# Performance work log

Measured on AMD Instinct MI355X. Metric: run time of the kernel, lower is better.

## Reference

```python
import jax, jax.numpy as jnp
import numpy as np

H = 16        # num_attention_heads
HS = 128      # head_size
ROT = 32      # rotary_ndims (partial RoPE, NeoX rotary_pct=0.25)
BASE = 10000.0


def _rope_cache(seq_len):
    inv_freq = 1.0 / (BASE ** (jnp.arange(0, ROT, 2, dtype=jnp.float32) / ROT))
    t = jnp.arange(seq_len, dtype=jnp.float32)
    freqs = jnp.outer(t, inv_freq)                      # [s, ROT/2]
    emb = jnp.concatenate([freqs, freqs], axis=-1)      # [s, ROT]
    return jnp.cos(emb), jnp.sin(emb)


def _rotate_half(x):
    x1, x2 = jnp.split(x, 2, axis=-1)
    return jnp.concatenate([-x2, x1], axis=-1)


def setup_inputs() -> dict:
    key = jax.random.key(0)
    k1, k2, k3 = jax.random.split(key, 3)
    B, S, D = 2, 2048, 2048
    hidden_states = jax.random.normal(k1, (B, S, D), dtype=jnp.float32)
    position_ids = jnp.broadcast_to(jnp.arange(S, dtype=jnp.int64 if jax.config.jax_enable_x64 else jnp.int32), (B, S))
    W_qkv = jax.random.normal(k2, (D, 3 * H * HS), dtype=jnp.float32) * 0.02
    b_qkv = jnp.zeros((3 * H * HS,), dtype=jnp.float32)
    W_dense = jax.random.normal(k3, (H * HS, D), dtype=jnp.float32) * 0.02
    b_dense = jnp.zeros((D,), dtype=jnp.float32)
    return {"hidden_states": hidden_states, "position_ids": position_ids,
            "W_qkv": W_qkv, "b_qkv": b_qkv, "W_dense": W_dense, "b_dense": b_dense}


def reference(hidden_states, position_ids, W_qkv, b_qkv, W_dense, b_dense):
    B, S, D = hidden_states.shape
    # fused QKV projection, NeoX layout: [b, s, h, 3*hs]
    qkv = (hidden_states @ W_qkv + b_qkv).reshape(B, S, H, 3 * HS)
    q = qkv[..., :HS]            # [b, s, h, hs]
    k = qkv[..., HS:2 * HS]
    v = qkv[..., 2 * HS:]

    # partial rotary embedding on first ROT dims
    cos, sin = _rope_cache(S)                       # [s, ROT]
    cos = cos[position_ids][:, :, None, :]          # [b, s, 1, ROT]
    sin = sin[position_ids][:, :, None, :]
    q_rot, q_pass = q[..., :ROT], q[..., ROT:]
    k_rot, k_pass = k[..., :ROT], k[..., ROT:]
    q_rot = q_rot * cos + _rotate_half(q_rot) * sin
    k_rot = k_rot * cos + _rotate_half(k_rot) * sin
    q = jnp.concatenate([q_rot, q_pass], axis=-1)
    k = jnp.concatenate([k_rot, k_pass], axis=-1)

    # scaled dot-product attention (no mask, as in the source SDPA call)
    scale = 1.0 / jnp.sqrt(jnp.asarray(HS, dtype=q.dtype))
    scores = jnp.einsum('bqhd,bkhd->bhqk', q, k) * scale   # [b, h, s, s]
    attn = jax.nn.softmax(scores, axis=-1)
    out = jnp.einsum('bhqk,bkhd->bqhd', attn, v)            # [b, s, h, hs]
    out = out.reshape(B, S, H * HS)                         # 'b h d n -> b d (h n)'
    return out @ W_dense + b_dense
```

## Files before the change

### kernel.cpp

```cpp
#include <hip/hip_runtime.h>

typedef short bf16x8 __attribute__((ext_vector_type(8)));
typedef float f32x4 __attribute__((ext_vector_type(4)));

#define S_LEN 2048
#define NHEAD 16
#define HSZ 128

__device__ __forceinline__ float bf2f(ushort u) {
    union { unsigned int i; float f; } x; x.i = ((unsigned int)u) << 16; return x.f;
}
__device__ __forceinline__ ushort f2bf(float f) {
    union { float f; unsigned int i; } x; x.f = f;
    unsigned int r = (x.i + 0x7FFFu + ((x.i >> 16) & 1u)) >> 16;
    return (ushort)r;
}

__device__ __forceinline__ void gload16(const ushort* g, ushort* l) {
    __builtin_amdgcn_global_load_lds(
        (const __attribute__((address_space(1))) unsigned int*)g,
        (__attribute__((address_space(3))) unsigned int*)l,
        16, 0, 0);
}

__global__ void cast_kernel(const float* __restrict__ in, ushort* __restrict__ out, int n4) {
    int i = blockIdx.x * 256 + threadIdx.x;
    if (i >= n4) return;
    float4 v = ((const float4*)in)[i];
    ushort4 r;
    r.x = f2bf(v.x); r.y = f2bf(v.y); r.z = f2bf(v.z); r.w = f2bf(v.w);
    ((ushort4*)out)[i] = r;
}

__global__ void transpose_cast(const float* __restrict__ W, ushort* __restrict__ WT,
                               int K, int N) {
    __shared__ float tile[32][33];
    int n = blockIdx.x * 32 + threadIdx.x;
    #pragma unroll
    for (int j = 0; j < 32; j += 8) {
        int k = blockIdx.y * 32 + threadIdx.y + j;
        tile[threadIdx.y + j][threadIdx.x] = W[(size_t)k * N + n];
    }
    __syncthreads();
    int k2 = blockIdx.y * 32 + threadIdx.x;
    #pragma unroll
    for (int j = 0; j < 32; j += 8) {
        int n2 = blockIdx.x * 32 + threadIdx.y + j;
        WT[(size_t)n2 * K + k2] = f2bf(tile[threadIdx.x][threadIdx.y + j]);
    }
}

template <int EPI>
__global__ __launch_bounds__(512, 2) void gemm256(
    const ushort* __restrict__ A, const ushort* __restrict__ Bt,
    const float* __restrict__ bias, float* __restrict__ Cout, int Kdim, int Ndim,
    ushort* __restrict__ q_out, ushort* __restrict__ k_out, ushort* __restrict__ v_out) {
    __shared__ __align__(16) ushort lA[4][8192];
    __shared__ __align__(16) ushort lB[4][8192];
    const int tid = threadIdx.x;
    const int m0 = blockIdx.y * 256, n0 = blockIdx.x * 256;
    const int lane = tid & 63, wid = tid >> 6;
    const int wm = wid >> 2, wn = wid & 3;
    const int lm = lane & 15, quad = lane >> 4;
    const int srow = tid >> 2;
    const int g8 = ((tid & 3) ^ ((tid >> 3) & 3)) * 8;
    const int wb = wid * 512;
    const int ch8 = (quad ^ ((lm >> 1) & 3)) * 8;
    const int aoff = (wm * 128 + lm) * 32 + ch8;
    const int boff = (wn * 64 + lm) * 32 + ch8;

    const ushort* pA = A + (size_t)(m0 + srow) * Kdim + g8;
    const ushort* pB = Bt + (size_t)(n0 + srow) * Kdim + g8;
    const size_t rhalf = (size_t)128 * Kdim;

    f32x4 acc[8][4];
    #pragma unroll
    for (int i = 0; i < 8; ++i)
        #pragma unroll
        for (int j = 0; j < 4; ++j) acc[i][j] = (f32x4){0.f, 0.f, 0.f, 0.f};

    const int T = Kdim >> 5;
    gload16(pA,              lA[0] + wb);
    gload16(pA + rhalf,      lA[0] + 4096 + wb);
    gload16(pB,              lB[0] + wb);
    gload16(pB + rhalf,      lB[0] + 4096 + wb);
    gload16(pA + 32,         lA[1] + wb);
    gload16(pA + 32 + rhalf, lA[1] + 4096 + wb);
    gload16(pB + 32,         lB[1] + wb);
    gload16(pB + 32 + rhalf, lB[1] + 4096 + wb);
    asm volatile("s_waitcnt vmcnt(4)" ::: "memory");
    asm volatile("s_barrier" ::: "memory");

    for (int t = 0; t < T; ++t) {
        const ushort* la = lA[t & 3];
        const ushort* lb = lB[t & 3];
        bf16x8 af[4], bfr[4];
        #pragma unroll
        for (int mt = 0; mt < 4; ++mt) af[mt] = *(const bf16x8*)(la + aoff + mt * 512);
        #pragma unroll
        for (int nt = 0; nt < 4; ++nt) bfr[nt] = *(const bf16x8*)(lb + boff + nt * 512);
        if (t + 2 < T) {
            ushort* da = lA[(t + 2) & 3];
            const ushort* sa = pA + (size_t)(t + 2) * 32;
            gload16(sa,         da + wb);
            gload16(sa + rhalf, da + 4096 + wb);
        }
        asm volatile("s_barrier" ::: "memory");
        __builtin_amdgcn_s_setprio(1);
        #pragma unroll
        for (int mt = 0; mt < 4; ++mt)
            #pragma unroll
            for (int nt = 0; nt < 4; ++nt)
                acc[mt][nt] = __builtin_amdgcn_mfma_f32_16x16x32_bf16(
                    af[mt], bfr[nt], acc[mt][nt], 0, 0, 0);
        __builtin_amdgcn_s_setprio(0);

        bf16x8 af2[4];
        #pragma unroll
        for (int mt = 0; mt < 4; ++mt) af2[mt] = *(const bf16x8*)(la + aoff + 2048 + mt * 512);
        if (t + 2 < T) {
            ushort* db = lB[(t + 2) & 3];
            const ushort* sb = pB + (size_t)(t + 2) * 32;
            gload16(sb,         db + wb);
            gload16(sb + rhalf, db + 4096 + wb);
        }
        asm volatile("s_barrier" ::: "memory");
        __builtin_amdgcn_s_setprio(1);
        #pragma unroll
        for (int mt = 0; mt < 4; ++mt)
            #pragma unroll
            for (int nt = 0; nt < 4; ++nt)
                acc[4 + mt][nt] = __builtin_amdgcn_mfma_f32_16x16x32_bf16(
                    af2[mt], bfr[nt], acc[4 + mt][nt], 0, 0, 0);
        __builtin_amdgcn_s_setprio(0);
        if (t + 2 < T) asm volatile("s_waitcnt vmcnt(4)" ::: "memory");
        else           asm volatile("s_waitcnt vmcnt(0)" ::: "memory");
        asm volatile("s_barrier" ::: "memory");
    }

    #pragma unroll
    for (int mt = 0; mt < 8; ++mt) {
        #pragma unroll
        for (int nt = 0; nt < 4; ++nt) {
            f32x4 c = acc[mt][nt];
            int gn = n0 + wn * 64 + nt * 16 + lm;
            float bv = bias[gn];
            #pragma unroll
            for (int i = 0; i < 4; ++i) {
                int gm = m0 + wm * 128 + mt * 16 + quad * 4 + i;
                float v = c[i] + bv;
                if (EPI == 0) {
                    int h = gn / 384, r = gn - h * 384;
                    int tt = r >> 7, d = r & 127;
                    int b = gm >> 11, s = gm & 2047;
                    ushort bb = f2bf(v);
                    if (tt == 0) {
                        q_out[((size_t)(b * NHEAD + h) * S_LEN + s) * HSZ + d] = bb;
                    } else if (tt == 1) {
                        k_out[((size_t)(b * NHEAD + h) * S_LEN + s) * HSZ + d] = bb;
                    } else {
                        v_out[((size_t)(b * NHEAD + h) * HSZ + d) * S_LEN + s] = bb;
                    }
                } else {
                    Cout[(size_t)gm * Ndim + gn] = v;
                }
            }
        }
    }
}

template <int EPI>
__global__ __launch_bounds__(256) void gemm128(
    const ushort* __restrict__ A, const ushort* __restrict__ Bt,
    const float* __restrict__ bias, float* __restrict__ Cout, int Kdim, int Ndim,
    ushort* __restrict__ q_out, ushort* __restrict__ k_out, ushort* __restrict__ v_out) {
    __shared__ __align__(16) ushort lA[2][128 * 32];
    __shared__ __align__(16) ushort lB[2][128 * 32];
    const int tid = threadIdx.x;
    const int m0 = blockIdx.y * 128, n0 = blockIdx.x * 128;
    const int lane = tid & 63, wid = tid >> 6;
    const int wm = wid >> 1, wn = wid & 1, lm = lane & 15, quad = lane >> 4;
    const int srow = tid >> 2;
    const int gc = (tid & 3) ^ ((tid >> 3) & 3);
    const int wb8 = (wid << 6) * 8;
    const int cs = (quad ^ ((lm >> 1) & 3)) * 8;

    const ushort* pA = A  + (size_t)(m0 + srow) * Kdim + gc * 8;
    const ushort* pB = Bt + (size_t)(n0 + srow) * Kdim + gc * 8;
    const size_t rhalf = (size_t)64 * Kdim;

    const int fA = (wm * 64 + lm) * 32;
    const int fB = (wn * 64 + lm) * 32;

    f32x4 acc[16];
    #pragma unroll
    for (int i = 0; i < 16; ++i) acc[i] = (f32x4){0.f, 0.f, 0.f, 0.f};

    const int T = Kdim >> 5;
    gload16(pA,         lA[0] + wb8);
    gload16(pA + rhalf, lA[0] + 2048 + wb8);
    gload16(pB,         lB[0] + wb8);
    gload16(pB + rhalf, lB[0] + 2048 + wb8);
    pA += 32; pB += 32;

    for (int t = 0; t < T; ++t) {
        __syncthreads();
        const ushort* la = lA[t & 1];
        const ushort* lb = lB[t & 1];
        if (t + 1 < T) {
            ushort* da = lA[(t + 1) & 1];
            ushort* db = lB[(t + 1) & 1];
            gload16(pA,         da + wb8);
            gload16(pA + rhalf, da + 2048 + wb8);
            gload16(pB,         db + wb8);
            gload16(pB + rhalf, db + 2048 + wb8);
            pA += 32; pB += 32;
        }
        bf16x8 af[4], bfr[4];
        #pragma unroll
        for (int t4 = 0; t4 < 4; ++t4) {
            af[t4]  = *(const bf16x8*)(la + fA + t4 * 512 + cs);
            bfr[t4] = *(const bf16x8*)(lb + fB + t4 * 512 + cs);
        }
        #pragma unroll
        for (int mt = 0; mt < 4; ++mt)
            #pragma unroll
            for (int nt = 0; nt < 4; ++nt)
                acc[mt * 4 + nt] = __builtin_amdgcn_mfma_f32_16x16x32_bf16(
                    af[mt], bfr[nt], acc[mt * 4 + nt], 0, 0, 0);
    }

    #pragma unroll
    for (int mt = 0; mt < 4; ++mt) {
        #pragma unroll
        for (int nt = 0; nt < 4; ++nt) {
            f32x4 c = acc[mt * 4 + nt];
            int gn = n0 + wn * 64 + nt * 16 + lm;
            float bv = bias[gn];
            #pragma unroll
            for (int i = 0; i < 4; ++i) {
                int gm = m0 + wm * 64 + mt * 16 + quad * 4 + i;
                float v = c[i] + bv;
                if (EPI == 0) {
                    int h = gn / 384, r = gn - h * 384;
                    int t = r >> 7, d = r & 127;
                    int b = gm >> 11, s = gm & 2047;
                    ushort bb = f2bf(v);
                    if (t == 0) {
                        q_out[((size_t)(b * NHEAD + h) * S_LEN + s) * HSZ + d] = bb;
                    } else if (t == 1) {
                        k_out[((size_t)(b * NHEAD + h) * S_LEN + s) * HSZ + d] = bb;
                    } else {
                        v_out[((size_t)(b * NHEAD + h) * HSZ + d) * S_LEN + s] = bb;
                    }
                } else {
                    Cout[(size_t)gm * Ndim + gn] = v;
                }
            }
        }
    }
}

__global__ void rope_kernel(ushort* __restrict__ Qr, ushort* __restrict__ Kr,
                            const int* __restrict__ pos_ids) {
    int idx = blockIdx.x * 256 + threadIdx.x;
    int j = idx & 15;
    int row = idx >> 4;
    int s = row & 2047;
    int bh = row >> 11;
    int b = bh >> 4;
    int pos = pos_ids[b * S_LEN + s];
    float inv = exp2f((float)j * -0.8304820237218405f);
    float th = (float)pos * inv;
    float sn, c;
    sincosf(th, &sn, &c);
    size_t base = (size_t)row * HSZ;
    {
        float x1 = bf2f(Qr[base + j]), x2 = bf2f(Qr[base + j + 16]);
        Qr[base + j]      = f2bf(x1 * c - x2 * sn);
        Qr[base + j + 16] = f2bf(x2 * c + x1 * sn);
    }
    {
        float x1 = bf2f(Kr[base + j]), x2 = bf2f(Kr[base + j + 16]);
        Kr[base + j]      = f2bf(x1 * c - x2 * sn);
        Kr[base + j + 16] = f2bf(x2 * c + x1 * sn);
    }
}

__global__ __launch_bounds__(256, 2) void attn_mfma(
    const ushort* __restrict__ Q, const ushort* __restrict__ K,
    const ushort* __restrict__ Vt, ushort* __restrict__ O) {
    __shared__ __align__(16) ushort lQ[128 * 136];
    __shared__ __align__(16) ushort lK[2][32 * 128];
    __shared__ __align__(16) ushort lVt[2][128 * 32];
    __shared__ __align__(16) ushort lP[4 * 32 * 40];

    const int tid = threadIdx.x;
    const int wid = tid >> 6, lane = tid & 63;
    const int L = lane & 15, quad = lane >> 4;
    const int bh = blockIdx.y;
    const int q0 = blockIdx.x * 128;
    const int wq0 = wid * 32;
    const size_t base = (size_t)bh * S_LEN * HSZ;
    const ushort* Qb = Q + base + (size_t)q0 * HSZ;
    const ushort* Kb = K + base;
    const ushort* Vb = Vt + base;
    ushort* lPw = lP + wid * (32 * 40);

    #pragma unroll
    for (int p = 0; p < 8; ++p) {
        int idx = tid + p * 256;
        int row = idx >> 4, ch = idx & 15;
        uint4 v = ((const uint4*)Qb)[idx];
        *(uint4*)(lQ + row * 136 + ch * 8) = v;
    }
    __syncthreads();

    bf16x8 qf[2][4];
    #pragma unroll
    for (int qs = 0; qs < 2; ++qs)
        #pragma unroll
        for (int dc = 0; dc < 4; ++dc)
            qf[qs][dc] = *(const bf16x8*)(lQ + (wq0 + qs * 16 + L) * 136 + dc * 32 + quad * 8);

    int kx[4];
    #pragma unroll
    for (int dc = 0; dc < 4; ++dc) kx[dc] = (((dc * 4 + quad) ^ (L & 7))) * 8;
    const int vx = (quad ^ ((L >> 1) & 3)) * 8;

    const int li0 = tid, li1 = tid + 256;
    const int ub0 = ((tid & 192)) * 8, ub1 = ((tid & 192) + 256) * 8;
    const int kr0 = li0 >> 4, kg0 = (li0 & 15) ^ (kr0 & 7);
    const int kr1 = li1 >> 4, kg1 = (li1 & 15) ^ (kr1 & 7);
    const int vd0 = li0 >> 2, vg0 = (li0 & 3) ^ ((vd0 >> 1) & 3);
    const int vd1 = li1 >> 2, vg1 = (li1 & 3) ^ ((vd1 >> 1) & 3);

    f32x4 acc_o[8][2];
    #pragma unroll
    for (int dt = 0; dt < 8; ++dt)
        #pragma unroll
        for (int qs = 0; qs < 2; ++qs) acc_o[dt][qs] = (f32x4){0.f, 0.f, 0.f, 0.f};
    float lacc[2] = {0.f, 0.f};
    const float scale = 0.08838834764831845f;
    const float SHIFT = 12.0f;

    {
        gload16(Kb + (size_t)kr0 * 128 + kg0 * 8, lK[0] + ub0);
        gload16(Kb + (size_t)kr1 * 128 + kg1 * 8, lK[0] + ub1);
        gload16(Vb + (size_t)vd0 * 2048 + vg0 * 8, lVt[0] + ub0);
        gload16(Vb + (size_t)vd1 * 2048 + vg1 * 8, lVt[0] + ub1);
    }

    for (int kt = 0; kt < S_LEN / 32; ++kt) {
        __syncthreads();
        const int cur = kt & 1;
        const ushort* lKc = lK[cur];
        const ushort* lVc = lVt[cur];
        if (kt + 1 < S_LEN / 32) {
            ushort* dK = lK[cur ^ 1];
            ushort* dV = lVt[cur ^ 1];
            int kb = (kt + 1) * 32;
            gload16(Kb + (size_t)(kb + kr0) * 128 + kg0 * 8, dK + ub0);
            gload16(Kb + (size_t)(kb + kr1) * 128 + kg1 * 8, dK + ub1);
            gload16(Vb + (size_t)vd0 * 2048 + kb + vg0 * 8, dV + ub0);
            gload16(Vb + (size_t)vd1 * 2048 + kb + vg1 * 8, dV + ub1);
        }

        f32x4 sa[2][2];
        #pragma unroll
        for (int t = 0; t < 2; ++t)
            #pragma unroll
            for (int qs = 0; qs < 2; ++qs) sa[t][qs] = (f32x4){0.f, 0.f, 0.f, 0.f};
        #pragma unroll
        for (int t = 0; t < 2; ++t)
            #pragma unroll
            for (int dc = 0; dc < 4; ++dc) {
                bf16x8 kf = *(const bf16x8*)(lKc + (t * 16 + L) * 128 + kx[dc]);
                sa[t][0] = __builtin_amdgcn_mfma_f32_16x16x32_bf16(kf, qf[0][dc], sa[t][0], 0, 0, 0);
                sa[t][1] = __builtin_amdgcn_mfma_f32_16x16x32_bf16(kf, qf[1][dc], sa[t][1], 0, 0, 0);
            }

        #pragma unroll
        for (int t = 0; t < 2; ++t)
            #pragma unroll
            for (int qs = 0; qs < 2; ++qs) {
                #pragma unroll
                for (int r = 0; r < 4; ++r) {
                    float pv = __expf(fmaf(sa[t][qs][r], scale, -SHIFT));
                    lacc[qs] += pv;
                    sa[t][qs][r] = pv;
                }
                ushort4 u;
                u.x = f2bf(sa[t][qs][0]);
                u.y = f2bf(sa[t][qs][1]);
                u.z = f2bf(sa[t][qs][2]);
                u.w = f2bf(sa[t][qs][3]);
                *(ushort4*)(lPw + (qs * 16 + L) * 40 + t * 16 + quad * 4) = u;
            }
        __asm__ volatile("s_waitcnt lgkmcnt(0)" ::: "memory");

        bf16x8 pf0 = *(const bf16x8*)(lPw + L * 40 + quad * 8);
        bf16x8 pf1 = *(const bf16x8*)(lPw + (16 + L) * 40 + quad * 8);
        #pragma unroll
        for (int dt = 0; dt < 8; ++dt) {
            bf16x8 vf = *(const bf16x8*)(lVc + (dt * 16 + L) * 32 + vx);
            acc_o[dt][0] = __builtin_amdgcn_mfma_f32_16x16x32_bf16(vf, pf0, acc_o[dt][0], 0, 0, 0);
            acc_o[dt][1] = __builtin_amdgcn_mfma_f32_16x16x32_bf16(vf, pf1, acc_o[dt][1], 0, 0, 0);
        }
    }

    const int b = bh >> 4, h = bh & 15;
    #pragma unroll
    for (int qs = 0; qs < 2; ++qs) {
        float l = lacc[qs];
        l += __shfl_xor(l, 16);
        l += __shfl_xor(l, 32);
        float inv = 1.f / l;
        size_t row = ((size_t)(b * S_LEN + q0 + wq0 + qs * 16 + L)) * (NHEAD * HSZ) + h * HSZ;
        #pragma unroll
        for (int dt = 0; dt < 8; ++dt) {
            ushort4 u;
            u.x = f2bf(acc_o[dt][qs][0] * inv);
            u.y = f2bf(acc_o[dt][qs][1] * inv);
            u.z = f2bf(acc_o[dt][qs][2] * inv);
            u.w = f2bf(acc_o[dt][qs][3] * inv);
            *(ushort4*)(O + row + dt * 16 + quad * 4) = u;
        }
    }
}

extern "C" void kernel_launch(void* const* d_in, const int* in_sizes, int n_in,
                              void* d_out, int out_size, void* d_ws, size_t ws_size,
                              hipStream_t stream) {
    const float* hidden = (const float*)d_in[0];
    const int*   pos    = (const int*)d_in[1];
    const float* Wqkv   = (const float*)d_in[2];
    const float* bqkv   = (const float*)d_in[3];
    const float* Wd     = (const float*)d_in[4];
    const float* bd     = (const float*)d_in[5];

    char* ws = (char*)d_ws;
    ushort* hA  = (ushort*)ws;
    ushort* WqT = (ushort*)(ws + 16777216ull);
    ushort* WdT = (ushort*)(ws + 41943040ull);
    ushort* Qb  = (ushort*)(ws + 50331648ull);
    ushort* Kb  = (ushort*)(ws + 67108864ull);
    ushort* Vb  = (ushort*)(ws + 83886080ull);

    cast_kernel<<<dim3(8192), dim3(256), 0, stream>>>(hidden, hA, 2097152);
    transpose_cast<<<dim3(192, 64), dim3(32, 8), 0, stream>>>(Wqkv, WqT, 2048, 6144);
    transpose_cast<<<dim3(64, 64), dim3(32, 8), 0, stream>>>(Wd, WdT, 2048, 2048);

    gemm256<0><<<dim3(24, 16), dim3(512), 0, stream>>>(hA, WqT, bqkv, nullptr, 2048, 6144,
                                                       Qb, Kb, Vb);
    rope_kernel<<<dim3(4096), dim3(256), 0, stream>>>(Qb, Kb, pos);

    ushort* Obuf = hA;
    attn_mfma<<<dim3(16, 32), dim3(256), 0, stream>>>(Qb, Kb, Vb, Obuf);

    gemm128<1><<<dim3(16, 32), dim3(256), 0, stream>>>(Obuf, WdT, bd, (float*)d_out,
                                                       2048, 2048, nullptr, nullptr, nullptr);
}
```

Baseline: 442.3 us.

## Restructure GEMM mainloop to 64-wide K tiles with four-phase ping-pong schedule

Measured after the change: 440.0 us. About the same (-0.5%).

```diff
diff --git a/kernel.cpp b/kernel.cpp
--- a/kernel.cpp
+++ b/kernel.cpp
@@ -22,6 +22,9 @@
         (__attribute__((address_space(3))) unsigned int*)l,
         16, 0, 0);
 }
+
+#define BAR()   asm volatile("s_barrier" ::: "memory")
+#define LGKM0() asm volatile("s_waitcnt lgkmcnt(0)" ::: "memory")
 
 __global__ void cast_kernel(const float* __restrict__ in, ushort* __restrict__ out, int n4) {
     int i = blockIdx.x * 256 + threadIdx.x;
@@ -55,23 +58,21 @@
     const ushort* __restrict__ A, const ushort* __restrict__ Bt,
     const float* __restrict__ bias, float* __restrict__ Cout, int Kdim, int Ndim,
     ushort* __restrict__ q_out, ushort* __restrict__ k_out, ushort* __restrict__ v_out) {
-    __shared__ __align__(16) ushort lA[4][8192];
-    __shared__ __align__(16) ushort lB[4][8192];
+    __shared__ __align__(16) ushort lds[65536];
     const int tid = threadIdx.x;
     const int m0 = blockIdx.y * 256, n0 = blockIdx.x * 256;
     const int lane = tid & 63, wid = tid >> 6;
     const int wm = wid >> 2, wn = wid & 3;
     const int lm = lane & 15, quad = lane >> 4;
+    const int cs = (quad ^ ((lm >> 1) & 3)) * 8;
+    const int aOff = wm * 8192 + lm * 32 + cs;
+    const int bOff = 16384 + (wn >> 1) * 8192 + (wn & 1) * 2048 + lm * 32 + cs;
     const int srow = tid >> 2;
-    const int g8 = ((tid & 3) ^ ((tid >> 3) & 3)) * 8;
-    const int wb = wid * 512;
-    const int ch8 = (quad ^ ((lm >> 1) & 3)) * 8;
-    const int aoff = (wm * 128 + lm) * 32 + ch8;
-    const int boff = (wn * 64 + lm) * 32 + ch8;
-
-    const ushort* pA = A + (size_t)(m0 + srow) * Kdim + g8;
-    const ushort* pB = Bt + (size_t)(n0 + srow) * Kdim + g8;
-    const size_t rhalf = (size_t)128 * Kdim;
+    const int xs8 = ((tid & 3) ^ ((tid >> 3) & 3)) * 8;
+    const ushort* pAs = A  + (size_t)(m0 + srow) * Kdim + xs8;
+    const ushort* pBs = Bt + (size_t)(n0 + srow) * Kdim + xs8;
+    const size_t hK = (size_t)128 * Kdim;
+    const int sw = wid * 512;
 
     f32x4 acc[8][4];
     #pragma unroll
@@ -79,63 +80,108 @@
         #pragma unroll
         for (int j = 0; j < 4; ++j) acc[i][j] = (f32x4){0.f, 0.f, 0.f, 0.f};
 
-    const int T = Kdim >> 5;
-    gload16(pA,              lA[0] + wb);
-    gload16(pA + rhalf,      lA[0] + 4096 + wb);
-    gload16(pB,              lB[0] + wb);
-    gload16(pB + rhalf,      lB[0] + 4096 + wb);
-    gload16(pA + 32,         lA[1] + wb);
-    gload16(pA + 32 + rhalf, lA[1] + 4096 + wb);
-    gload16(pB + 32,         lB[1] + wb);
-    gload16(pB + 32 + rhalf, lB[1] + 4096 + wb);
-    asm volatile("s_waitcnt vmcnt(4)" ::: "memory");
-    asm volatile("s_barrier" ::: "memory");
+    const int T = Kdim >> 6;
+
+    auto stageB = [&](int t) {
+        ushort* b = lds + (t & 1) * 32768 + 16384 + sw;
+        const ushort* g = pBs + (size_t)t * 64;
+        gload16(g,            b);
+        gload16(g + 32,       b + 4096);
+        gload16(g + hK,       b + 8192);
+        gload16(g + hK + 32,  b + 12288);
+    };
+    auto stageA = [&](int t) {
+        ushort* b = lds + (t & 1) * 32768 + sw;
+        const ushort* g = pAs + (size_t)t * 64;
+        gload16(g,            b);
+        gload16(g + 32,       b + 4096);
+        gload16(g + hK,       b + 8192);
+        gload16(g + hK + 32,  b + 12288);
+    };
+
+    stageB(0); stageA(0); stageB(1); stageA(1);
+    asm volatile("s_waitcnt vmcnt(8)" ::: "memory");
+    BAR();
 
     for (int t = 0; t < T; ++t) {
-        const ushort* la = lA[t & 3];
-        const ushort* lb = lB[t & 3];
-        bf16x8 af[4], bfr[4];
-        #pragma unroll
-        for (int mt = 0; mt < 4; ++mt) af[mt] = *(const bf16x8*)(la + aoff + mt * 512);
-        #pragma unroll
-        for (int nt = 0; nt < 4; ++nt) bfr[nt] = *(const bf16x8*)(lb + boff + nt * 512);
-        if (t + 2 < T) {
-            ushort* da = lA[(t + 2) & 3];
-            const ushort* sa = pA + (size_t)(t + 2) * 32;
-            gload16(sa,         da + wb);
-            gload16(sa + rhalf, da + 4096 + wb);
-        }
-        asm volatile("s_barrier" ::: "memory");
+        const ushort* la = lds + (t & 1) * 32768 + aOff;
+        const ushort* lb = lds + (t & 1) * 32768 + bOff;
+        const bool pf = (t + 2 < T);
+
+        bf16x8 afL[4][2], bfL[2][2];
+        #pragma unroll
+        for (int mt = 0; mt < 4; ++mt)
+            #pragma unroll
+            for (int ks = 0; ks < 2; ++ks)
+                afL[mt][ks] = *(const bf16x8*)(la + ks * 4096 + mt * 512);
+        #pragma unroll
+        for (int nt = 0; nt < 2; ++nt)
+            #pragma unroll
+            for (int ks = 0; ks < 2; ++ks)
+                bfL[nt][ks] = *(const bf16x8*)(lb + ks * 4096 + nt * 512);
+        BAR(); LGKM0();
         __builtin_amdgcn_s_setprio(1);
         #pragma unroll
         for (int mt = 0; mt < 4; ++mt)
             #pragma unroll
-            for (int nt = 0; nt < 4; ++nt)
-                acc[mt][nt] = __builtin_amdgcn_mfma_f32_16x16x32_bf16(
-                    af[mt], bfr[nt], acc[mt][nt], 0, 0, 0);
+            for (int nt = 0; nt < 2; ++nt) {
+                acc[mt][nt] = __builtin_amdgcn_mfma_f32_16x16x32_bf16(afL[mt][0], bfL[nt][0], acc[mt][nt], 0, 0, 0);
+                acc[mt][nt] = __builtin_amdgcn_mfma_f32_16x16x32_bf16(afL[mt][1], bfL[nt][1], acc[mt][nt], 0, 0, 0);
+            }
         __builtin_amdgcn_s_setprio(0);
-
-        bf16x8 af2[4];
-        #pragma unroll
-        for (int mt = 0; mt < 4; ++mt) af2[mt] = *(const bf16x8*)(la + aoff + 2048 + mt * 512);
-        if (t + 2 < T) {
-            ushort* db = lB[(t + 2) & 3];
-            const ushort* sb = pB + (size_t)(t + 2) * 32;
-            gload16(sb,         db + wb);
-            gload16(sb + rhalf, db + 4096 + wb);
-        }
-        asm volatile("s_barrier" ::: "memory");
+        BAR();
+
+        bf16x8 bfH[2][2];
+        #pragma unroll
+        for (int nt = 0; nt < 2; ++nt)
+            #pragma unroll
+            for (int ks = 0; ks < 2; ++ks)
+                bfH[nt][ks] = *(const bf16x8*)(lb + ks * 4096 + (nt + 2) * 512);
+        BAR(); LGKM0();
         __builtin_amdgcn_s_setprio(1);
         #pragma unroll
         for (int mt = 0; mt < 4; ++mt)
             #pragma unroll
-            for (int nt = 0; nt < 4; ++nt)
-                acc[4 + mt][nt] = __builtin_amdgcn_mfma_f32_16x16x32_bf16(
-                    af2[mt], bfr[nt], acc[4 + mt][nt], 0, 0, 0);
+            for (int nt = 0; nt < 2; ++nt) {
+                acc[mt][nt + 2] = __builtin_amdgcn_mfma_f32_16x16x32_bf16(afL[mt][0], bfH[nt][0], acc[mt][nt + 2], 0, 0, 0);
+                acc[mt][nt + 2] = __builtin_amdgcn_mfma_f32_16x16x32_bf16(afL[mt][1], bfH[nt][1], acc[mt][nt + 2], 0, 0, 0);
+            }
         __builtin_amdgcn_s_setprio(0);
-        if (t + 2 < T) asm volatile("s_waitcnt vmcnt(4)" ::: "memory");
-        else           asm volatile("s_waitcnt vmcnt(0)" ::: "memory");
-        asm volatile("s_barrier" ::: "memory");
+        BAR();
+
+        bf16x8 afH[4][2];
+        #pragma unroll
+        for (int mt = 0; mt < 4; ++mt)
+            #pragma unroll
+            for (int ks = 0; ks < 2; ++ks)
+                afH[mt][ks] = *(const bf16x8*)(la + ks * 4096 + (mt + 4) * 512);
+        if (pf) stageB(t + 2);
+        BAR(); LGKM0();
+        __builtin_amdgcn_s_setprio(1);
+        #pragma unroll
+        for (int mt = 0; mt < 4; ++mt)
+            #pragma unroll
+            for (int nt = 0; nt < 2; ++nt) {
+                acc[mt + 4][nt] = __builtin_amdgcn_mfma_f32_16x16x32_bf16(afH[mt][0], bfL[nt][0], acc[mt + 4][nt], 0, 0, 0);
+                acc[mt + 4][nt] = __builtin_amdgcn_mfma_f32_16x16x32_bf16(afH[mt][1], bfL[nt][1], acc[mt + 4][nt], 0, 0, 0);
+            }
+        __builtin_amdgcn_s_setprio(0);
+        BAR();
+
+        if (pf) stageA(t + 2);
+        BAR();
+        __builtin_amdgcn_s_setprio(1);
+        #pragma unroll
+        for (int mt = 0; mt < 4; ++mt)
+            #pragma unroll
+            for (int nt = 0; nt < 2; ++nt) {
+                acc[mt + 4][nt + 2] = __builtin_amdgcn_mfma_f32_16x16x32_bf16(afH[mt][0], bfH[nt][0], acc[mt + 4][nt + 2], 0, 0, 0);
+                acc[mt + 4][nt + 2] = __builtin_amdgcn_mfma_f32_16x16x32_bf16(afH[mt][1], bfH[nt][1], acc[mt + 4][nt + 2], 0, 0, 0);
+            }
+        __builtin_amdgcn_s_setprio(0);
+        if (pf) asm volatile("s_waitcnt vmcnt(8)" ::: "memory");
+        else    asm volatile("s_waitcnt vmcnt(0)" ::: "memory");
+        BAR();
     }
 
     #pragma unroll
```
